# Optimization experiments

Hardware: AMD Instinct MI355X
Metric: run time of the kernel (lower is better)

Reference implementation:

```python
import jax, jax.numpy as jnp
import numpy as np

N_QUBITS = 12
N_LAYERS = 4
BATCH = 4096
DIM = 2 ** N_QUBITS  # 4096


def _apply_1q(state, U, q):
    """Apply 2x2 complex gate U to qubit q. state: (B,) + (2,)*n, wire 0 = MSB (axis q+1)."""
    state = jnp.moveaxis(state, q + 1, -1)
    state = state @ U.T
    return jnp.moveaxis(state, -1, q + 1)


def _apply_cnot(state, c, t):
    """CNOT with control c, target t: flip target amplitudes where control bit == 1."""
    flipped = jnp.flip(state, axis=t + 1)
    shape = [2 if i == c + 1 else 1 for i in range(state.ndim)]
    ctrl = jnp.arange(2).reshape(shape)
    return jnp.where(ctrl == 1, flipped, state)


def setup_inputs() -> dict:
    key = jax.random.key(0)
    k1, k2 = jax.random.split(key)
    x = jax.random.normal(k1, (BATCH, DIM), dtype=jnp.float32)
    weights = jax.random.normal(k2, (N_LAYERS, N_QUBITS, 2), dtype=jnp.float32) * 0.1
    return {"x": x, "weights": weights}


def reference(x, weights):
    n, L = N_QUBITS, N_LAYERS
    B = x.shape[0]
    # AmplitudeEmbedding with normalize=True
    norm = jnp.linalg.norm(x, axis=-1, keepdims=True)
    state = (x / norm).astype(jnp.complex64).reshape((B,) + (2,) * n)
    for layer in range(L):
        for q in range(n):
            ty = weights[layer, q, 0]
            tz = weights[layer, q, 1]
            c, s = jnp.cos(ty / 2), jnp.sin(ty / 2)
            em = jnp.exp(-0.5j * tz.astype(jnp.complex64))  # e^{-i tz/2}
            ep = jnp.exp(+0.5j * tz.astype(jnp.complex64))
            # U = RZ(tz) @ RY(ty), fused single 2x2 gate per qubit
            U = jnp.stack([
                jnp.stack([c * em, -s * em]),
                jnp.stack([s * ep, c * ep]),
            ]).astype(jnp.complex64)
            state = _apply_1q(state, U, q)
        for q in range(n - 1):
            state = _apply_cnot(state, q, q + 1)
        if n > 2:
            state = _apply_cnot(state, n - 1, 0)
    probs = jnp.abs(state) ** 2  # (B,) + (2,)*n, float32
    reduce_axes = tuple(range(1, probs.ndim))
    outs = []
    for q in range(n):
        shape = [2 if i == q + 1 else 1 for i in range(probs.ndim)]
        sign = jnp.array([1.0, -1.0], dtype=probs.dtype).reshape(shape)
        outs.append(jnp.sum(probs * sign, axis=reduce_axes))
    return jnp.stack(outs, axis=-1)  # (B, n_qubits) <Z_q> expvals
```

## Files before the change

### kernel.cpp

```cpp
#include <hip/hip_runtime.h>

#define NQ   12
#define DIM  4096
#define NL   4
#define BLK  256

typedef unsigned short u16;
typedef unsigned int   u32;
typedef float f2 __attribute__((ext_vector_type(2)));

struct L12 { u16 b[NQ]; };

static constexpr u32 lap(const L12& A, u32 x){ u32 r=0; for(int p=0;p<NQ;++p) if((x>>p)&1u) r^=A.b[p]; return r; }
static constexpr L12 lcomp(const L12& A, const L12& B){ L12 r{}; for(int p=0;p<NQ;++p) r.b[p]=(u16)lap(A,(u32)B.b[p]); return r; }
static constexpr L12 lident(){ L12 r{}; for(int p=0;p<NQ;++p) r.b[p]=(u16)(1u<<p); return r; }

static constexpr u32 applyT(u32 i){
  i ^= ((i>>0)&1u) << 11;
  for(int q=10;q>=0;--q){ int pc=11-q, pt=10-q; i ^= ((i>>pc)&1u) << pt; }
  return i;
}
static constexpr L12 lT(){ L12 t{}; for(int p=0;p<NQ;++p) t.b[p]=(u16)applyT(1u<<p); return t; }

static constexpr L12 linv(const L12& A){
  u16 v[NQ]; u16 u[NQ];
  for(int p=0;p<NQ;++p){ v[p]=A.b[p]; u[p]=(u16)(1u<<p); }
  for(int t=0;t<NQ;++t){
    int p=t; while(!((v[p]>>t)&1u)) ++p;
    u16 tv=v[p]; v[p]=v[t]; v[t]=tv; u16 tu=u[p]; u[p]=u[t]; u[t]=tu;
    for(int k=0;k<NQ;++k) if(k!=t && ((v[k]>>t)&1u)){ v[k]^=v[t]; u[k]^=u[t]; }
  }
  L12 r{}; for(int p=0;p<NQ;++p) r.b[p]=u[p]; return r;
}
static constexpr L12 ltr(const L12& A){
  L12 r{}; for(int p=0;p<NQ;++p) for(int q=0;q<NQ;++q) if((A.b[p]>>q)&1u) r.b[q]=(u16)(r.b[q]|(1u<<p));
  return r;
}
static constexpr int cpop(u32 v){ int n=0; while(v){ n+=(int)(v&1u); v>>=1; } return n; }

struct Tables {
  u16 cm[12][16];
  u16 wg[12][4];
  u16 sp[12][4];
  u16 wexp[NQ];
};

static constexpr Tables make_tables(){
  Tables tb{};
  const L12 T   = lT();
  const L12 Tit = ltr(linv(T));
  L12 A = lident();
  L12 W = lident();
  for(int l=0;l<NL;++l){
    for(int g=0;g<3;++g){
      const int st = l*3+g;
      u16 mm[4]={0,0,0,0};
      for(int i=0;i<4;++i){ mm[i]=A.b[4*g+i]; tb.wg[st][i]=W.b[4*g+i]; }
      u32 ech[4]={0,0,0,0}; int piv[4]={0,0,0,0};
      for(int i=0;i<4;++i){
        u32 v=mm[i];
        for(int k=0;k<i;++k) if((v>>piv[k])&1u) v^=ech[k];
        int t2=11; while(!((v>>t2)&1u)) --t2;
        piv[i]=t2; ech[i]=v;
      }
      for(int a2=0;a2<4;++a2) for(int b2=a2+1;b2<4;++b2)
        if(piv[b2]<piv[a2]){ int tt=piv[a2]; piv[a2]=piv[b2]; piv[b2]=tt; }
      for(int i=0;i<4;++i) tb.sp[st][i]=(u16)piv[i];
      for(int c=0;c<16;++c){ u32 m=0; for(int i=0;i<4;++i) if((c>>i)&1) m^=mm[i]; tb.cm[st][c]=(u16)m; }
    }
    A = lcomp(A, T);
    W = lcomp(W, Tit);
  }
  for(int p=0;p<NQ;++p) tb.wexp[p]=W.b[p];
  return tb;
}

__device__ constexpr Tables TB = make_tables();

static constexpr u16 UIMG[12] = {1,2,4,8, 3,5,6,7, 9,10,11,13};

static constexpr u32 swz(u32 j){
  u32 f=0;
  for(int k=4;k<12;++k) if((j>>k)&1u) f ^= (u32)UIMG[k];
  return j ^ (f & 15u);
}

struct Derived {
  u32 lane_c[12][8];
  u32 smb[12][4];
  u32 scmb[12][16];
  u32 g0lane[8];
  u32 u11lane[8];
  u32 u11smb[4];
  u16 pm[12];
  u16 mu[12];
};

static constexpr Derived make_derived(){
  const Tables tb = make_tables();
  Derived d{};
  for(int st=0; st<12; ++st){
    bool isp[12]={false,false,false,false,false,false,false,false,false,false,false,false};
    for(int i=0;i<4;++i) isp[tb.sp[st][i]]=true;
    int np[8]; int nn=0;
    for(int p=0;p<12;++p) if(!isp[p]) np[nn++]=p;
    int best=-1;
    for(int ms=0; ms<256; ++ms){
      int pc=0; for(int k=0;k<8;++k) pc+=(ms>>k)&1;
      if(pc!=6) continue;
      u16 bas[4]={0,0,0,0}; int r=0;
      for(int k=0;k<8;++k){
        if(!((ms>>k)&1)) continue;
        u16 x=(u16)(UIMG[np[k]]&15);
        while(x){
          int hb=3; while(!((x>>hb)&1)) --hb;
          if(bas[hb]) x=(u16)(x^bas[hb]);
          else { bas[hb]=x; ++r; x=0; }
        }
      }
      if(r==4){ best=ms; break; }
    }
    if(best<0) best=0x3F;
    int pos[8]; int lo=0, hi=6;
    for(int k=0;k<8;++k){ if((best>>k)&1) pos[lo++]=np[k]; else pos[hi++]=np[k]; }
    for(int k=0;k<8;++k){
      const u32 addr = swz(1u<<pos[k])<<3;
      u32 nib=0;
      for(int i=0;i<4;++i) nib |= (u32)((tb.wg[st][i]>>pos[k])&1u)<<i;
      d.lane_c[st][k] = addr | (nib<<28);
      if(st==0)  d.g0lane[k]  = 1u<<pos[k];
      if(st==11) d.u11lane[k] = 1u<<pos[k];
    }
    for(int i=0;i<4;++i)  d.smb[st][i]  = swz((u32)tb.cm[st][1<<i])<<3;
    for(int c=0;c<16;++c) d.scmb[st][c] = swz((u32)tb.cm[st][c])<<3;
    if(st==11) for(int i=0;i<4;++i) d.u11smb[i] = (u32)tb.cm[11][1<<i];
  }
  for(int q=0;q<12;++q){
    d.pm[q] = tb.wexp[11-q];
    u32 m=0;
    for(int i=0;i<4;++i) m |= (u32)(cpop((u32)tb.cm[11][1u<<i] & (u32)tb.wexp[11-q])&1)<<i;
    d.mu[q]=(u16)m;
  }
  return d;
}

__device__ constexpr Derived DV = make_derived();

template<int ST, bool WITHW>
__device__ __forceinline__ void gates(f2 (&a)[16], const float4* __restrict__ gw){
#pragma unroll
  for(int i=0;i<4;++i){
    const float4 g = gw[ST*4+i];
    const f2 mt = {-g.x, -g.x};
    const f2 sy = { g.y,  g.y};
#pragma unroll
    for(int c=0;c<16;++c){
      if((c>>i)&1) continue;
      const int c1 = c|(1<<i);
      f2 u = __builtin_elementwise_fma(mt, a[c1], a[c]);
      f2 v = __builtin_elementwise_fma(sy, u, a[c1]);
      a[c] = __builtin_elementwise_fma(mt, v, u);
      if(WITHW){
        const float t = fmaf(-g.z, v.y, v.x);
        v.y = fmaf( g.w, t, v.y);
        v.x = fmaf(-g.z, v.y, t);
      }
      a[c1]=v;
    }
  }
}

template<int ST, bool WITHW>
__device__ __forceinline__ void mid_step(const u32* msk, char* lds, const float4* __restrict__ gw){
  u32 acc=0;
#pragma unroll
  for(int k=0;k<8;++k) acc ^= DV.lane_c[ST][k]&msk[k];
  const u32 nib = acc>>28;
  u32 base = acc & 0x0FFFFFFFu;
#pragma unroll
  for(int i=0;i<4;++i) base ^= DV.smb[ST][i] & (0u-((nib>>i)&1u));
  u32 ad[16]; f2 a[16];
#pragma unroll
  for(int c=0;c<16;++c){
    ad[c] = base ^ DV.scmb[ST][c];
    a[c] = *(const f2*)(lds+ad[c]);
  }
  gates<ST,WITHW>(a,gw);
#pragma unroll
  for(int c=0;c<16;++c){ *(f2*)(lds+ad[c]) = a[c]; }
  __syncthreads();
}

__global__ void prep_kernel(const float* __restrict__ w, float4* __restrict__ gw){
  const int t = threadIdx.x;
  if(t < NL*NQ){
    const int l=t/NQ, p=t%NQ, q=(NQ-1)-p;
    const float ty=w[(l*NQ+q)*2+0], tz=w[(l*NQ+q)*2+1];
    gw[t]=make_float4(tanf(0.25f*ty), sinf(0.5f*ty), tanf(0.5f*tz), sinf(tz));
  }
}

__global__ __launch_bounds__(BLK, 5) void qsim_kernel(const float* __restrict__ x,
                                                      const float4* __restrict__ gw,
                                                      float* __restrict__ out)
{
  __shared__ f2 st2[DIM];
  char* lds = (char*)st2;
  const int tid = threadIdx.x;
  const int bb  = blockIdx.x;

  u32 msk[8];
#pragma unroll
  for(int k=0;k<8;++k) msk[k]=0u-((u32)(tid>>k)&1u);

  u32 rep0=0, acc0=0;
#pragma unroll
  for(int k=0;k<8;++k){ rep0 ^= DV.g0lane[k]&msk[k]; acc0 ^= DV.lane_c[0][k]&msk[k]; }
  const u32 base0 = acc0 & 0x0FFFFFFFu;

  f2 a[16];
  const float* xr = x + (size_t)bb*DIM + rep0;
#pragma unroll
  for(int s=0;s<4;++s){
    const float4 v = *reinterpret_cast<const float4*>(xr + 4*s);
    a[4*s+0]=(f2){v.x,0.f}; a[4*s+1]=(f2){v.y,0.f};
    a[4*s+2]=(f2){v.z,0.f}; a[4*s+3]=(f2){v.w,0.f};
  }
  gates<0,true>(a,gw);
#pragma unroll
  for(int c=0;c<16;++c){ *(f2*)(lds + (base0 ^ DV.scmb[0][c])) = a[c]; }
  __syncthreads();

  mid_step<1,true >(msk,lds,gw);
  mid_step<2,true >(msk,lds,gw);
  mid_step<3,true >(msk,lds,gw);
  mid_step<4,true >(msk,lds,gw);
  mid_step<5,true >(msk,lds,gw);
  mid_step<6,true >(msk,lds,gw);
  mid_step<7,true >(msk,lds,gw);
  mid_step<8,true >(msk,lds,gw);
  mid_step<9,false>(msk,lds,gw);
  mid_step<10,false>(msk,lds,gw);

  {
    u32 acc=0, urep=0;
#pragma unroll
    for(int k=0;k<8;++k){ acc ^= DV.lane_c[11][k]&msk[k]; urep ^= DV.u11lane[k]&msk[k]; }
    const u32 nib = acc>>28;
    u32 base = acc & 0x0FFFFFFFu;
#pragma unroll
    for(int i=0;i<4;++i){ const u32 mi=0u-((nib>>i)&1u); base ^= DV.smb[11][i]&mi; urep ^= DV.u11smb[i]&mi; }
#pragma unroll
    for(int c=0;c<16;++c){
      a[c] = *(const f2*)(lds + (base ^ DV.scmb[11][c]));
    }
    gates<11,false>(a,gw);

    float pr[16];
#pragma unroll
    for(int c=0;c<16;++c) pr[c]=fmaf(a[c].x,a[c].x, a[c].y*a[c].y);
#pragma unroll
    for(int b=1;b<16;b<<=1){
#pragma unroll
      for(int c=0;c<16;++c){
        if(c&b) continue;
        const float u=pr[c], v=pr[c|b];
        pr[c]=u+v; pr[c|b]=u-v;
      }
    }
    float accq[12];
#pragma unroll
    for(int q=0;q<12;++q){
      const u32 sb = ((u32)__popc(urep & (u32)DV.pm[q]) & 1u)<<31;
      accq[q]=__uint_as_float(__float_as_uint(pr[DV.mu[q]])^sb);
    }
    float nrm2 = pr[0];
#pragma unroll
    for(int o=32;o;o>>=1){
      nrm2 += __shfl_xor(nrm2,o);
#pragma unroll
      for(int q=0;q<12;++q) accq[q]+=__shfl_xor(accq[q],o);
    }
    __syncthreads();
    float* wredf = (float*)lds;
    const int wid=tid>>6;
    if((tid&63)==0){
#pragma unroll
      for(int q=0;q<12;++q) wredf[wid*13+q]=accq[q];
      wredf[wid*13+12]=nrm2;
    }
    __syncthreads();
    if(tid<NQ){
      const float s0=wredf[0*13+tid]+wredf[1*13+tid]+wredf[2*13+tid]+wredf[3*13+tid];
      const float sn=wredf[0*13+12]+wredf[1*13+12]+wredf[2*13+12]+wredf[3*13+12];
      out[(size_t)bb*NQ+tid]=s0/sn;
    }
  }
}

extern "C" void kernel_launch(void* const* d_in, const int* in_sizes, int n_in,
                              void* d_out, int out_size, void* d_ws, size_t ws_size,
                              hipStream_t stream) {
  const float* x = (const float*)d_in[0];
  const float* w = (const float*)d_in[1];
  float* out = (float*)d_out;
  float4* gw = (float4*)d_ws;
  const int B = in_sizes[0] / DIM;
  prep_kernel<<<1, 64, 0, stream>>>(w, gw);
  qsim_kernel<<<B, BLK, 0, stream>>>(x, gw, out);
}
```

Baseline: 107.0 us.

## Regroup gates into 3-qubit stages with 512 threads per block

```diff
diff --git a/kernel.cpp b/kernel.cpp
--- a/kernel.cpp
+++ b/kernel.cpp
@@ -3,12 +3,15 @@
 #define NQ   12
 #define DIM  4096
 #define NL   4
-#define BLK  256
+#define BLK  512
 
 typedef unsigned short u16;
 typedef unsigned int   u32;
 typedef float f2 __attribute__((ext_vector_type(2)));
 
+static constexpr int par(u32 v){ return __builtin_popcount(v)&1; }
+static constexpr int hb(u16 v){ for(int i=11;i>=0;--i) if((v>>i)&1u) return i; return -1; }
+
 struct L12 { u16 b[NQ]; };
 
 static constexpr u32 lap(const L12& A, u32 x){ u32 r=0; for(int p=0;p<NQ;++p) if((x>>p)&1u) r^=A.b[p]; return r; }
@@ -17,13 +20,13 @@
 
 static constexpr u32 applyT(u32 i){
   i ^= ((i>>0)&1u) << 11;
-  for(int q=10;q>=0;--q){ int pc=11-q, pt=10-q; i ^= ((i>>pc)&1u) << pt; }
+  for(int q=10;q>=0;--q){ int pc2=11-q, pt=10-q; i ^= ((i>>pc2)&1u) << pt; }
   return i;
 }
 static constexpr L12 lT(){ L12 t{}; for(int p=0;p<NQ;++p) t.b[p]=(u16)applyT(1u<<p); return t; }
 
 static constexpr L12 linv(const L12& A){
-  u16 v[NQ]; u16 u[NQ];
+  u16 v[NQ]={}; u16 u[NQ]={};
   for(int p=0;p<NQ;++p){ v[p]=A.b[p]; u[p]=(u16)(1u<<p); }
   for(int t=0;t<NQ;++t){
     int p=t; while(!((v[p]>>t)&1u)) ++p;
@@ -36,12 +39,10 @@
   L12 r{}; for(int p=0;p<NQ;++p) for(int q=0;q<NQ;++q) if((A.b[p]>>q)&1u) r.b[q]=(u16)(r.b[q]|(1u<<p));
   return r;
 }
-static constexpr int cpop(u32 v){ int n=0; while(v){ n+=(int)(v&1u); v>>=1; } return n; }
 
 struct Tables {
   u16 cm[12][16];
   u16 wg[12][4];
-  u16 sp[12][4];
   u16 wexp[NQ];
 };
 
@@ -56,16 +57,6 @@
       const int st = l*3+g;
       u16 mm[4]={0,0,0,0};
       for(int i=0;i<4;++i){ mm[i]=A.b[4*g+i]; tb.wg[st][i]=W.b[4*g+i]; }
-      u32 ech[4]={0,0,0,0}; int piv[4]={0,0,0,0};
-      for(int i=0;i<4;++i){
-        u32 v=mm[i];
-        for(int k=0;k<i;++k) if((v>>piv[k])&1u) v^=ech[k];
-        int t2=11; while(!((v>>t2)&1u)) --t2;
-        piv[i]=t2; ech[i]=v;
-      }
-      for(int a2=0;a2<4;++a2) for(int b2=a2+1;b2<4;++b2)
-        if(piv[b2]<piv[a2]){ int tt=piv[a2]; piv[a2]=piv[b2]; piv[b2]=tt; }
-      for(int i=0;i<4;++i) tb.sp[st][i]=(u16)piv[i];
       for(int c=0;c<16;++c){ u32 m=0; for(int i=0;i<4;++i) if((c>>i)&1) m^=mm[i]; tb.cm[st][c]=(u16)m; }
     }
     A = lcomp(A, T);
@@ -75,133 +66,230 @@
   return tb;
 }
 
-__device__ constexpr Tables TB = make_tables();
-
 static constexpr u16 UIMG[12] = {1,2,4,8, 3,5,6,7, 9,10,11,13};
-
 static constexpr u32 swz(u32 j){
   u32 f=0;
   for(int k=4;k<12;++k) if((j>>k)&1u) f ^= (u32)UIMG[k];
   return j ^ (f & 15u);
 }
 
-struct Derived {
-  u32 lane_c[12][8];
-  u32 smb[12][4];
-  u32 scmb[12][16];
-  u32 g0lane[8];
-  u32 u11lane[8];
-  u32 u11smb[4];
-  u16 pm[12];
-  u16 mu[12];
+struct Ech { u16 s[12]; };
+static constexpr u16 ered(const Ech& e, u16 x){
+  while(x){
+    const int lb=hb(x);
+    if(e.s[lb]) x=(u16)(x^e.s[lb]); else break;
+  }
+  return x;
+}
+static constexpr bool eadd(Ech& e, u16 x){
+  x=ered(e,x); if(!x) return false;
+  e.s[hb(x)]=x; return true;
+}
+
+struct Trip {
+  u32 lane_c[9];
+  u32 raw9[9];
+  u32 smb[3];
+  u32 rawm[3];
+  u32 scmb[8];
+  u32 cinv[3];
+  u32 rho[3];
+  bool cok;
 };
 
-static constexpr Derived make_derived(){
+static constexpr Trip make_trip(int t){
+  Trip r{};
   const Tables tb = make_tables();
-  Derived d{};
-  for(int st=0; st<12; ++st){
-    bool isp[12]={false,false,false,false,false,false,false,false,false,false,false,false};
-    for(int i=0;i<4;++i) isp[tb.sp[st][i]]=true;
-    int np[8]; int nn=0;
-    for(int p=0;p<12;++p) if(!isp[p]) np[nn++]=p;
-    int best=-1;
-    for(int ms=0; ms<256; ++ms){
-      int pc=0; for(int k=0;k<8;++k) pc+=(ms>>k)&1;
-      if(pc!=6) continue;
-      u16 bas[4]={0,0,0,0}; int r=0;
-      for(int k=0;k<8;++k){
-        if(!((ms>>k)&1)) continue;
-        u16 x=(u16)(UIMG[np[k]]&15);
-        while(x){
-          int hb=3; while(!((x>>hb)&1)) --hb;
-          if(bas[hb]) x=(u16)(x^bas[hb]);
-          else { bas[hb]=x; ++r; x=0; }
+  u16 M[3]={}, w[3]={};
+  for(int j=0;j<3;++j){
+    const int g=3*t+j, st=g>>2, qi=g&3;
+    M[j]=tb.cm[st][(u32)1<<qi]; w[j]=tb.wg[st][qi];
+  }
+  Ech em{};
+  for(int j=0;j<3;++j) eadd(em,M[j]);
+  bool isp[12]={};
+  for(int b2=0;b2<12;++b2) if(em.s[b2]) isp[b2]=true;
+  int np[12]={}; int nn=0;
+  for(int p=0;p<12;++p) if(!isp[p]) np[nn++]=p;
+  int s0=0,s1=1,s2=2,s3=3; bool found=false;
+  for(int i0=0;i0<nn&&!found;++i0)for(int i1=i0+1;i1<nn&&!found;++i1)
+  for(int i2=i1+1;i2<nn&&!found;++i2)for(int i3=i2+1;i3<nn&&!found;++i3){
+    u16 img[4]={(u16)(swz((u32)1<<np[i0])&15u),(u16)(swz((u32)1<<np[i1])&15u),
+                (u16)(swz((u32)1<<np[i2])&15u),(u16)(swz((u32)1<<np[i3])&15u)};
+    u16 bas[4]={0,0,0,0}; int rk=0;
+    for(int ii=0;ii<4;++ii){
+      u16 x=img[ii];
+      while(x){
+        int hbx=3; while(hbx>0 && !((x>>hbx)&1)) --hbx;
+        if(bas[hbx]) x=(u16)(x^bas[hbx]); else { bas[hbx]=x; ++rk; x=0; }
+      }
+    }
+    if(rk==4){ s0=i0;s1=i1;s2=i2;s3=i3; found=true; }
+  }
+  int ord[9]={}; ord[0]=s0;ord[1]=s1;ord[2]=s2;ord[3]=s3;
+  int rp=4;
+  for(int j=0;j<nn;++j){ if(j!=s0&&j!=s1&&j!=s2&&j!=s3) ord[rp++]=j; }
+  for(int k=0;k<9;++k){
+    const int f=np[ord[k]];
+    u32 nib=0;
+    for(int i=0;i<3;++i) nib |= (u32)((w[i]>>f)&1u)<<i;
+    r.lane_c[k]=(swz((u32)1<<f)<<3)|(nib<<28);
+    r.raw9[k]=(u32)1<<f;
+  }
+  for(int k=0;k<3;++k){ r.smb[k]=swz((u32)M[k])<<3; r.rawm[k]=(u32)M[k]; }
+  for(int c=0;c<8;++c){
+    u32 m=0;
+    for(int j=0;j<3;++j) if((c>>j)&1) m^=(u32)M[j];
+    r.scmb[c]=swz(m)<<3;
+  }
+  u32 beta[3]={};
+  for(int i=0;i<3;++i){ u32 row=0; for(int k=0;k<3;++k) row|=(u32)par((u32)(M[k]&w[i]))<<k; beta[i]=row; }
+  u32 rows[3]={ beta[0]|(1u<<3), beta[1]|(2u<<3), beta[2]|(4u<<3) };
+  bool ok=true;
+  for(int col=0;col<3;++col){
+    int pv=-1;
+    for(int rr=col;rr<3;++rr) if((rows[rr]>>col)&1u){pv=rr;break;}
+    if(pv<0){ok=false;break;}
+    u32 tt=rows[col]; rows[col]=rows[pv]; rows[pv]=tt;
+    for(int rr=0;rr<3;++rr) if(rr!=col&&((rows[rr]>>col)&1u)) rows[rr]^=rows[col];
+  }
+  r.cok=ok;
+  if(ok) for(int k=0;k<3;++k) r.cinv[k]=(rows[k]>>3)&7u;
+  for(int i=0;i<3;++i){
+    u32 m=0;
+    for(int c=0;c<8;++c){
+      int v=0;
+      for(int j=0;j<3;++j) if(j!=i && ((c>>j)&1)) v ^= (int)((beta[i]>>j)&1u);
+      m |= (u32)v<<c;
+    }
+    r.rho[i]=m;
+  }
+  return r;
+}
+
+static constexpr Trip TRIPS[16] = {
+  make_trip(0), make_trip(1), make_trip(2), make_trip(3),
+  make_trip(4), make_trip(5), make_trip(6), make_trip(7),
+  make_trip(8), make_trip(9), make_trip(10), make_trip(11),
+  make_trip(12), make_trip(13), make_trip(14), make_trip(15)
+};
+
+struct RD { u16 pm[12]; u16 mu[12]; };
+static constexpr RD make_rd(){
+  RD r{};
+  const Tables tb=make_tables();
+  u16 M[3]={};
+  for(int j=0;j<3;++j) M[j]=tb.cm[11][(u32)1<<(1+j)];
+  for(int q=0;q<12;++q){
+    r.pm[q]=tb.wexp[11-q];
+    u32 m=0;
+    for(int j=0;j<3;++j) m|=(u32)par((u32)(M[j]&tb.wexp[11-q]))<<j;
+    r.mu[q]=(u16)m;
+  }
+  return r;
+}
+static constexpr RD RDT = make_rd();
+
+__device__ __forceinline__ float fx(float a, u32 m){ return __uint_as_float(__float_as_uint(a)^m); }
+
+template<int TI, int J>
+__device__ __forceinline__ void one_gate(f2 (&a)[8], const float4* __restrict__ gw,
+                                         const float4* __restrict__ gwH, u32 nib){
+  constexpr int G = 3*TI+J;
+  constexpr bool WITHW = (G < 36);
+  const float4 g = gw[G];
+  if constexpr (TRIPS[TI].cok){
+#pragma unroll
+    for(int c=0;c<8;++c){
+      if((c>>J)&1) continue;
+      const int c1=c|(1<<J);
+      const int p = ((TRIPS[TI].rho[J]>>c)&1u) ? c1 : c;
+      const int q = ((TRIPS[TI].rho[J]>>c)&1u) ? c : c1;
+      f2 u,v;
+      u.x=fmaf(-g.x,a[q].x,a[p].x); u.y=fmaf(-g.x,a[q].y,a[p].y);
+      v.x=fmaf( g.y,u.x,a[q].x);    v.y=fmaf( g.y,u.y,a[q].y);
+      a[p].x=fmaf(-g.x,v.x,u.x);    a[p].y=fmaf(-g.x,v.y,u.y);
+      if(WITHW){ const float tt=fmaf(-g.z,v.y,v.x); v.y=fmaf(g.w,tt,v.y); v.x=fmaf(-g.z,v.y,tt); }
+      a[q]=v;
+    }
+  } else {
+    const u32 Rm = ((nib>>J)&1u)<<31;
+    const float tg=fx(g.x,Rm), sg=fx(g.y,Rm);
+    float t2=0.f, s2=0.f;
+    if constexpr (WITHW){
+      const float4 h=gwH[G];
+      t2=fx(h.x,Rm^0x80000000u); s2=fx(h.y,Rm^0x80000000u);
+    }
+#pragma unroll
+    for(int c=0;c<8;++c){
+      if((c>>J)&1) continue;
+      const int c1=c|(1<<J);
+      if(((TRIPS[TI].rho[J]>>c)&1u)==0){
+        f2 u,v;
+        u.x=fmaf(-tg,a[c1].x,a[c].x); u.y=fmaf(-tg,a[c1].y,a[c].y);
+        v.x=fmaf( sg,u.x,a[c1].x);    v.y=fmaf( sg,u.y,a[c1].y);
+        a[c].x=fmaf(-tg,v.x,u.x);     a[c].y=fmaf(-tg,v.y,u.y);
+        a[c1]=v;
+        if(WITHW){
+          float tt=fmaf(-t2,a[c].y,a[c].x);   a[c].y=fmaf( s2,tt,a[c].y);   a[c].x=fmaf(-t2,a[c].y,tt);
+          tt=fmaf( t2,a[c1].y,a[c1].x);       a[c1].y=fmaf(-s2,tt,a[c1].y); a[c1].x=fmaf( t2,a[c1].y,tt);
+        }
+      } else {
+        f2 u,v;
+        u.x=fmaf( tg,a[c1].x,a[c].x); u.y=fmaf( tg,a[c1].y,a[c].y);
+        v.x=fmaf(-sg,u.x,a[c1].x);    v.y=fmaf(-sg,u.y,a[c1].y);
+        a[c].x=fmaf( tg,v.x,u.x);     a[c].y=fmaf( tg,v.y,u.y);
+        a[c1]=v;
+        if(WITHW){
+          float tt=fmaf( t2,a[c].y,a[c].x);   a[c].y=fmaf(-s2,tt,a[c].y);   a[c].x=fmaf( t2,a[c].y,tt);
+          tt=fmaf(-t2,a[c1].y,a[c1].x);       a[c1].y=fmaf( s2,tt,a[c1].y); a[c1].x=fmaf(-t2,a[c1].y,tt);
         }
       }
-      if(r==4){ best=ms; break; }
-    }
-    if(best<0) best=0x3F;
-    int pos[8]; int lo=0, hi=6;
-    for(int k=0;k<8;++k){ if((best>>k)&1) pos[lo++]=np[k]; else pos[hi++]=np[k]; }
-    for(int k=0;k<8;++k){
-      const u32 addr = swz(1u<<pos[k])<<3;
-      u32 nib=0;
-      for(int i=0;i<4;++i) nib |= (u32)((tb.wg[st][i]>>pos[k])&1u)<<i;
-      d.lane_c[st][k] = addr | (nib<<28);
-      if(st==0)  d.g0lane[k]  = 1u<<pos[k];
-      if(st==11) d.u11lane[k] = 1u<<pos[k];
-    }
-    for(int i=0;i<4;++i)  d.smb[st][i]  = swz((u32)tb.cm[st][1<<i])<<3;
-    for(int c=0;c<16;++c) d.scmb[st][c] = swz((u32)tb.cm[st][c])<<3;
-    if(st==11) for(int i=0;i<4;++i) d.u11smb[i] = (u32)tb.cm[11][1<<i];
-  }
-  for(int q=0;q<12;++q){
-    d.pm[q] = tb.wexp[11-q];
-    u32 m=0;
-    for(int i=0;i<4;++i) m |= (u32)(cpop((u32)tb.cm[11][1u<<i] & (u32)tb.wexp[11-q])&1)<<i;
-    d.mu[q]=(u16)m;
-  }
-  return d;
-}
-
-__device__ constexpr Derived DV = make_derived();
-
-template<int ST, bool WITHW>
-__device__ __forceinline__ void gates(f2 (&a)[16], const float4* __restrict__ gw){
-#pragma unroll
-  for(int i=0;i<4;++i){
-    const float4 g = gw[ST*4+i];
-    const f2 mt = {-g.x, -g.x};
-    const f2 sy = { g.y,  g.y};
-#pragma unroll
-    for(int c=0;c<16;++c){
-      if((c>>i)&1) continue;
-      const int c1 = c|(1<<i);
-      f2 u = __builtin_elementwise_fma(mt, a[c1], a[c]);
-      f2 v = __builtin_elementwise_fma(sy, u, a[c1]);
-      a[c] = __builtin_elementwise_fma(mt, v, u);
-      if(WITHW){
-        const float t = fmaf(-g.z, v.y, v.x);
-        v.y = fmaf( g.w, t, v.y);
-        v.x = fmaf(-g.z, v.y, t);
-      }
-      a[c1]=v;
-    }
-  }
-}
-
-template<int ST, bool WITHW>
-__device__ __forceinline__ void mid_step(const u32* msk, char* lds, const float4* __restrict__ gw){
+    }
+  }
+}
+
+template<int TI>
+__device__ __forceinline__ void trip_mid(const u32* msk, char* lds,
+                                         const float4* __restrict__ gw,
+                                         const float4* __restrict__ gwH){
   u32 acc=0;
 #pragma unroll
-  for(int k=0;k<8;++k) acc ^= DV.lane_c[ST][k]&msk[k];
+  for(int k=0;k<9;++k) acc ^= TRIPS[TI].lane_c[k]&msk[k];
   const u32 nib = acc>>28;
   u32 base = acc & 0x0FFFFFFFu;
-#pragma unroll
-  for(int i=0;i<4;++i) base ^= DV.smb[ST][i] & (0u-((nib>>i)&1u));
-  u32 ad[16]; f2 a[16];
-#pragma unroll
-  for(int c=0;c<16;++c){
-    ad[c] = base ^ DV.scmb[ST][c];
-    a[c] = *(const f2*)(lds+ad[c]);
-  }
-  gates<ST,WITHW>(a,gw);
-#pragma unroll
-  for(int c=0;c<16;++c){ *(f2*)(lds+ad[c]) = a[c]; }
+  if constexpr (TRIPS[TI].cok){
+#pragma unroll
+    for(int k=0;k<3;++k){
+      const u32 sk=(u32)(__popc(TRIPS[TI].cinv[k]&nib)&1);
+      base ^= TRIPS[TI].smb[k]&(0u-sk);
+    }
+  }
+  f2 a[8]; u32 ad[8];
+#pragma unroll
+  for(int c=0;c<8;++c){ ad[c]=base^TRIPS[TI].scmb[c]; a[c]=*(const f2*)(lds+ad[c]); }
+  one_gate<TI,0>(a,gw,gwH,nib);
+  one_gate<TI,1>(a,gw,gwH,nib);
+  one_gate<TI,2>(a,gw,gwH,nib);
+#pragma unroll
+  for(int c=0;c<8;++c){ *(f2*)(lds+ad[c])=a[c]; }
   __syncthreads();
 }
 
-__global__ void prep_kernel(const float* __restrict__ w, float4* __restrict__ gw){
+__global__ void prep_kernel(const float* __restrict__ w, float4* __restrict__ gw,
+                            float4* __restrict__ gwH){
   const int t = threadIdx.x;
   if(t < NL*NQ){
     const int l=t/NQ, p=t%NQ, q=(NQ-1)-p;
     const float ty=w[(l*NQ+q)*2+0], tz=w[(l*NQ+q)*2+1];
     gw[t]=make_float4(tanf(0.25f*ty), sinf(0.5f*ty), tanf(0.5f*tz), sinf(tz));
-  }
-}
-
-__global__ __launch_bounds__(BLK, 5) void qsim_kernel(const float* __restrict__ x,
+    gwH[t]=make_float4(tanf(0.25f*tz), sinf(0.5f*tz), 0.f, 0.f);
+  }
+}
+
+__global__ __launch_bounds__(BLK, 8) void qsim_kernel(const float* __restrict__ x,
                                                       const float4* __restrict__ gw,
+                                                      const float4* __restrict__ gwH,
                                                       float* __restrict__ out)
 {
   __shared__ f2 st2[DIM];
@@ -209,60 +297,72 @@
   const int tid = threadIdx.x;
   const int bb  = blockIdx.x;
 
-  u32 msk[8];
-#pragma unroll
-  for(int k=0;k<8;++k) msk[k]=0u-((u32)(tid>>k)&1u);
-
-  u32 rep0=0, acc0=0;
-#pragma unroll
-  for(int k=0;k<8;++k){ rep0 ^= DV.g0lane[k]&msk[k]; acc0 ^= DV.lane_c[0][k]&msk[k]; }
-  const u32 base0 = acc0 & 0x0FFFFFFFu;
-
-  f2 a[16];
-  const float* xr = x + (size_t)bb*DIM + rep0;
-#pragma unroll
-  for(int s=0;s<4;++s){
-    const float4 v = *reinterpret_cast<const float4*>(xr + 4*s);
-    a[4*s+0]=(f2){v.x,0.f}; a[4*s+1]=(f2){v.y,0.f};
-    a[4*s+2]=(f2){v.z,0.f}; a[4*s+3]=(f2){v.w,0.f};
-  }
-  gates<0,true>(a,gw);
-#pragma unroll
-  for(int c=0;c<16;++c){ *(f2*)(lds + (base0 ^ DV.scmb[0][c])) = a[c]; }
-  __syncthreads();
-
-  mid_step<1,true >(msk,lds,gw);
-  mid_step<2,true >(msk,lds,gw);
-  mid_step<3,true >(msk,lds,gw);
-  mid_step<4,true >(msk,lds,gw);
-  mid_step<5,true >(msk,lds,gw);
-  mid_step<6,true >(msk,lds,gw);
-  mid_step<7,true >(msk,lds,gw);
-  mid_step<8,true >(msk,lds,gw);
-  mid_step<9,false>(msk,lds,gw);
-  mid_step<10,false>(msk,lds,gw);
+  u32 msk[9];
+#pragma unroll
+  for(int k=0;k<9;++k) msk[k]=0u-((u32)(tid>>k)&1u);
+
+  {
+    u32 acc=0, raw=0;
+#pragma unroll
+    for(int k=0;k<9;++k){ acc ^= TRIPS[0].lane_c[k]&msk[k]; raw ^= TRIPS[0].raw9[k]&msk[k]; }
+    const u32 base = acc & 0x0FFFFFFFu;
+    f2 a[8];
+    const float* xr = x + (size_t)bb*DIM + raw;
+    const float4 v0 = *reinterpret_cast<const float4*>(xr);
+    const float4 v1 = *reinterpret_cast<const float4*>(xr+4);
+    a[0]=(f2){v0.x,0.f}; a[1]=(f2){v0.y,0.f}; a[2]=(f2){v0.z,0.f}; a[3]=(f2){v0.w,0.f};
+    a[4]=(f2){v1.x,0.f}; a[5]=(f2){v1.y,0.f}; a[6]=(f2){v1.z,0.f}; a[7]=(f2){v1.w,0.f};
+    one_gate<0,0>(a,gw,gwH,0u);
+    one_gate<0,1>(a,gw,gwH,0u);
+    one_gate<0,2>(a,gw,gwH,0u);
+#pragma unroll
+    for(int c=0;c<8;++c){ *(f2*)(lds + (base^TRIPS[0].scmb[c])) = a[c]; }
+    __syncthreads();
+  }
+
+  trip_mid<1 >(msk,lds,gw,gwH);
+  trip_mid<2 >(msk,lds,gw,gwH);
+  trip_mid<3 >(msk,lds,gw,gwH);
+  trip_mid<4 >(msk,lds,gw,gwH);
+  trip_mid<5 >(msk,lds,gw,gwH);
+  trip_mid<6 >(msk,lds,gw,gwH);
+  trip_mid<7 >(msk,lds,gw,gwH);
+  trip_mid<8 >(msk,lds,gw,gwH);
+  trip_mid<9 >(msk,lds,gw,gwH);
+  trip_mid<10>(msk,lds,gw,gwH);
+  trip_mid<11>(msk,lds,gw,gwH);
+  trip_mid<12>(msk,lds,gw,gwH);
+  trip_mid<13>(msk,lds,gw,gwH);
+  trip_mid<14>(msk,lds,gw,gwH);
 
   {
     u32 acc=0, urep=0;
 #pragma unroll
-    for(int k=0;k<8;++k){ acc ^= DV.lane_c[11][k]&msk[k]; urep ^= DV.u11lane[k]&msk[k]; }
+    for(int k=0;k<9;++k){ acc ^= TRIPS[15].lane_c[k]&msk[k]; urep ^= TRIPS[15].raw9[k]&msk[k]; }
     const u32 nib = acc>>28;
     u32 base = acc & 0x0FFFFFFFu;
-#pragma unroll
-    for(int i=0;i<4;++i){ const u32 mi=0u-((nib>>i)&1u); base ^= DV.smb[11][i]&mi; urep ^= DV.u11smb[i]&mi; }
-#pragma unroll
-    for(int c=0;c<16;++c){
-      a[c] = *(const f2*)(lds + (base ^ DV.scmb[11][c]));
-    }
-    gates<11,false>(a,gw);
-
-    float pr[16];
-#pragma unroll
-    for(int c=0;c<16;++c) pr[c]=fmaf(a[c].x,a[c].x, a[c].y*a[c].y);
-#pragma unroll
-    for(int b=1;b<16;b<<=1){
-#pragma unroll
-      for(int c=0;c<16;++c){
+    if constexpr (TRIPS[15].cok){
+#pragma unroll
+      for(int k=0;k<3;++k){
+        const u32 sk=(u32)(__popc(TRIPS[15].cinv[k]&nib)&1);
+        const u32 mi=0u-sk;
+        base ^= TRIPS[15].smb[k]&mi; urep ^= TRIPS[15].rawm[k]&mi;
+      }
+    }
+    f2 a[8];
+#pragma unroll
+    for(int c=0;c<8;++c){ a[c]=*(const f2*)(lds + (base^TRIPS[15].scmb[c])); }
+    one_gate<15,0>(a,gw,gwH,nib);
+    one_gate<15,1>(a,gw,gwH,nib);
+    one_gate<15,2>(a,gw,gwH,nib);
+
+    float pr[8];
+#pragma unroll
+    for(int c=0;c<8;++c) pr[c]=fmaf(a[c].x,a[c].x, a[c].y*a[c].y);
+#pragma unroll
+    for(int b=1;b<8;b<<=1){
+#pragma unroll
+      for(int c=0;c<8;++c){
         if(c&b) continue;
         const float u=pr[c], v=pr[c|b];
         pr[c]=u+v; pr[c|b]=u-v;
@@ -271,8 +371,8 @@
     float accq[12];
 #pragma unroll
     for(int q=0;q<12;++q){
-      const u32 sb = ((u32)__popc(urep & (u32)DV.pm[q]) & 1u)<<31;
-      accq[q]=__uint_as_float(__float_as_uint(pr[DV.mu[q]])^sb);
+      const u32 sb = ((u32)__popc(urep & (u32)RDT.pm[q]) & 1u)<<31;
+      accq[q]=__uint_as_float(__float_as_uint(pr[RDT.mu[q]])^sb);
     }
     float nrm2 = pr[0];
 #pragma unroll
@@ -291,8 +391,9 @@
     }
     __syncthreads();
     if(tid<NQ){
-      const float s0=wredf[0*13+tid]+wredf[1*13+tid]+wredf[2*13+tid]+wredf[3*13+tid];
-      const float sn=wredf[0*13+12]+wredf[1*13+12]+wredf[2*13+12]+wredf[3*13+12];
+      float s0=0.f, sn=0.f;
+#pragma unroll
+      for(int wv=0;wv<8;++wv){ s0+=wredf[wv*13+tid]; sn+=wredf[wv*13+12]; }
       out[(size_t)bb*NQ+tid]=s0/sn;
     }
   }
@@ -304,8 +405,9 @@
   const float* x = (const float*)d_in[0];
   const float* w = (const float*)d_in[1];
   float* out = (float*)d_out;
-  float4* gw = (float4*)d_ws;
+  float4* gw  = (float4*)d_ws;
+  float4* gwH = gw + NL*NQ;
   const int B = in_sizes[0] / DIM;
-  prep_kernel<<<1, 64, 0, stream>>>(w, gw);
-  qsim_kernel<<<B, BLK, 0, stream>>>(x, gw, out);
-}
+  prep_kernel<<<1, 64, 0, stream>>>(w, gw, gwH);
+  qsim_kernel<<<B, BLK, 0, stream>>>(x, gw, gwH, out);
+}
```

After: 121.9 us. +13.9%, slower.

## Split LDS state into separate real/imag planes with new bank-aware lane mapping

Applied to the files above, without the earlier changes.

```diff
diff --git a/kernel.cpp b/kernel.cpp
--- a/kernel.cpp
+++ b/kernel.cpp
@@ -4,6 +4,7 @@
 #define DIM  4096
 #define NL   4
 #define BLK  256
+#define IMOFF 16384
 
 typedef unsigned short u16;
 typedef unsigned int   u32;
@@ -11,19 +12,20 @@
 
 struct L12 { u16 b[NQ]; };
 
+static constexpr int pcnt(u32 v){ return __builtin_popcount(v); }
 static constexpr u32 lap(const L12& A, u32 x){ u32 r=0; for(int p=0;p<NQ;++p) if((x>>p)&1u) r^=A.b[p]; return r; }
 static constexpr L12 lcomp(const L12& A, const L12& B){ L12 r{}; for(int p=0;p<NQ;++p) r.b[p]=(u16)lap(A,(u32)B.b[p]); return r; }
 static constexpr L12 lident(){ L12 r{}; for(int p=0;p<NQ;++p) r.b[p]=(u16)(1u<<p); return r; }
 
 static constexpr u32 applyT(u32 i){
   i ^= ((i>>0)&1u) << 11;
-  for(int q=10;q>=0;--q){ int pc=11-q, pt=10-q; i ^= ((i>>pc)&1u) << pt; }
+  for(int q=10;q>=0;--q){ int pc2=11-q, pt=10-q; i ^= ((i>>pc2)&1u) << pt; }
   return i;
 }
 static constexpr L12 lT(){ L12 t{}; for(int p=0;p<NQ;++p) t.b[p]=(u16)applyT(1u<<p); return t; }
 
 static constexpr L12 linv(const L12& A){
-  u16 v[NQ]; u16 u[NQ];
+  u16 v[NQ]={}; u16 u[NQ]={};
   for(int p=0;p<NQ;++p){ v[p]=A.b[p]; u[p]=(u16)(1u<<p); }
   for(int t=0;t<NQ;++t){
     int p=t; while(!((v[p]>>t)&1u)) ++p;
@@ -36,7 +38,6 @@
   L12 r{}; for(int p=0;p<NQ;++p) for(int q=0;q<NQ;++q) if((A.b[p]>>q)&1u) r.b[q]=(u16)(r.b[q]|(1u<<p));
   return r;
 }
-static constexpr int cpop(u32 v){ int n=0; while(v){ n+=(int)(v&1u); v>>=1; } return n; }
 
 struct Tables {
   u16 cm[12][16];
@@ -102,43 +103,50 @@
   for(int st=0; st<12; ++st){
     bool isp[12]={false,false,false,false,false,false,false,false,false,false,false,false};
     for(int i=0;i<4;++i) isp[tb.sp[st][i]]=true;
-    int np[8]; int nn=0;
+    int np[8]={}; int nn=0;
     for(int p=0;p<12;++p) if(!isp[p]) np[nn++]=p;
-    int best=-1;
-    for(int ms=0; ms<256; ++ms){
-      int pc=0; for(int k=0;k<8;++k) pc+=(ms>>k)&1;
-      if(pc!=6) continue;
-      u16 bas[4]={0,0,0,0}; int r=0;
-      for(int k=0;k<8;++k){
-        if(!((ms>>k)&1)) continue;
-        u16 x=(u16)(UIMG[np[k]]&15);
-        while(x){
-          int hb=3; while(!((x>>hb)&1)) --hb;
-          if(bas[hb]) x=(u16)(x^bas[hb]);
-          else { bas[hb]=x; ++r; x=0; }
+    int s4=-1;
+    for(int j=0;j<8;++j) if(np[j]==4) s4=j;
+    int bestmask=-1;
+    for(int avoid=1; avoid>=0 && bestmask<0; --avoid){
+      for(int ms=0; ms<256 && bestmask<0; ++ms){
+        if(pcnt((u32)ms)!=4) continue;
+        if(avoid==1 && s4>=0 && ((ms>>s4)&1)) continue;
+        u16 bas[4]={0,0,0,0}; int rk=0;
+        for(int k=0;k<8;++k){
+          if(!((ms>>k)&1)) continue;
+          u16 x=(u16)(swz(1u<<np[k])&15u);
+          while(x){
+            int hbx=3; while(hbx>0 && !((x>>hbx)&1)) --hbx;
+            if(bas[hbx]) x=(u16)(x^bas[hbx]);
+            else { bas[hbx]=x; ++rk; x=0; }
+          }
         }
+        if(rk==4) bestmask=ms;
       }
-      if(r==4){ best=ms; break; }
-    }
-    if(best<0) best=0x3F;
-    int pos[8]; int lo=0, hi=6;
-    for(int k=0;k<8;++k){ if((best>>k)&1) pos[lo++]=np[k]; else pos[hi++]=np[k]; }
+    }
+    if(bestmask<0) bestmask=0x0F;
+    bool used[8]={};
+    int pos[8]={}; int lo=0;
+    for(int k=0;k<8;++k) if((bestmask>>k)&1){ pos[lo++]=np[k]; used[k]=true; }
+    if(s4>=0 && !used[s4]){ pos[lo++]=np[s4]; used[s4]=true; }
+    for(int k=0;k<8;++k) if(!used[k]){ pos[lo++]=np[k]; }
     for(int k=0;k<8;++k){
-      const u32 addr = swz(1u<<pos[k])<<3;
+      const u32 addr = swz(1u<<pos[k])<<2;
       u32 nib=0;
       for(int i=0;i<4;++i) nib |= (u32)((tb.wg[st][i]>>pos[k])&1u)<<i;
       d.lane_c[st][k] = addr | (nib<<28);
       if(st==0)  d.g0lane[k]  = 1u<<pos[k];
       if(st==11) d.u11lane[k] = 1u<<pos[k];
     }
-    for(int i=0;i<4;++i)  d.smb[st][i]  = swz((u32)tb.cm[st][1<<i])<<3;
-    for(int c=0;c<16;++c) d.scmb[st][c] = swz((u32)tb.cm[st][c])<<3;
+    for(int i=0;i<4;++i)  d.smb[st][i]  = swz((u32)tb.cm[st][1<<i])<<2;
+    for(int c=0;c<16;++c) d.scmb[st][c] = swz((u32)tb.cm[st][c])<<2;
     if(st==11) for(int i=0;i<4;++i) d.u11smb[i] = (u32)tb.cm[11][1<<i];
   }
   for(int q=0;q<12;++q){
     d.pm[q] = tb.wexp[11-q];
     u32 m=0;
-    for(int i=0;i<4;++i) m |= (u32)(cpop((u32)tb.cm[11][1u<<i] & (u32)tb.wexp[11-q])&1)<<i;
+    for(int i=0;i<4;++i) m |= (u32)(pcnt((u32)tb.cm[11][1u<<i] & (u32)tb.wexp[11-q])&1)<<i;
     d.mu[q]=(u16)m;
   }
   return d;
@@ -183,11 +191,15 @@
 #pragma unroll
   for(int c=0;c<16;++c){
     ad[c] = base ^ DV.scmb[ST][c];
-    a[c] = *(const f2*)(lds+ad[c]);
+    a[c].x = *(const float*)(lds+ad[c]);
+    a[c].y = *(const float*)(lds+ad[c]+IMOFF);
   }
   gates<ST,WITHW>(a,gw);
 #pragma unroll
-  for(int c=0;c<16;++c){ *(f2*)(lds+ad[c]) = a[c]; }
+  for(int c=0;c<16;++c){
+    *(float*)(lds+ad[c])       = a[c].x;
+    *(float*)(lds+ad[c]+IMOFF) = a[c].y;
+  }
   __syncthreads();
 }
 
@@ -204,7 +216,7 @@
                                                       const float4* __restrict__ gw,
                                                       float* __restrict__ out)
 {
-  __shared__ f2 st2[DIM];
+  __shared__ float st2[2*DIM];
   char* lds = (char*)st2;
   const int tid = threadIdx.x;
   const int bb  = blockIdx.x;
@@ -228,7 +240,11 @@
   }
   gates<0,true>(a,gw);
 #pragma unroll
-  for(int c=0;c<16;++c){ *(f2*)(lds + (base0 ^ DV.scmb[0][c])) = a[c]; }
+  for(int c=0;c<16;++c){
+    const u32 ad = base0 ^ DV.scmb[0][c];
+    *(float*)(lds+ad)       = a[c].x;
+    *(float*)(lds+ad+IMOFF) = a[c].y;
+  }
   __syncthreads();
 
   mid_step<1,true >(msk,lds,gw);
@@ -252,7 +268,9 @@
     for(int i=0;i<4;++i){ const u32 mi=0u-((nib>>i)&1u); base ^= DV.smb[11][i]&mi; urep ^= DV.u11smb[i]&mi; }
 #pragma unroll
     for(int c=0;c<16;++c){
-      a[c] = *(const f2*)(lds + (base ^ DV.scmb[11][c]));
+      const u32 ad = base ^ DV.scmb[11][c];
+      a[c].x = *(const float*)(lds+ad);
+      a[c].y = *(const float*)(lds+ad+IMOFF);
     }
     gates<11,false>(a,gw);
 
```

New measurement: 126.1 us. +17.8%, slower.
